# Performance work log

Hardware: AMD Instinct MI355X
Metric: run time of the kernel (lower is better)

Reference implementation:

```python
import jax, jax.numpy as jnp
import numpy as np

B, S, E, D = 4, 2048, 1024, 64  # batch, seq, embed_size, low-rank d; dv = E

def setup_inputs() -> dict:
    key = jax.random.key(0)
    ks = jax.random.split(key, 10)
    sc_e = 1.0 / np.sqrt(E)
    sc_d = 1.0 / np.sqrt(D)
    return {
        "x": jax.random.normal(ks[0], (B, S, E), jnp.float32),
        "y": jax.random.normal(ks[1], (B, S, E), jnp.float32),
        "Wq": jax.random.uniform(ks[2], (D, E), jnp.float32, -sc_e, sc_e),
        "bq": jax.random.uniform(ks[3], (D,), jnp.float32, -sc_e, sc_e),
        "Wk": jax.random.uniform(ks[4], (D, E), jnp.float32, -sc_e, sc_e),
        "bk": jax.random.uniform(ks[5], (D,), jnp.float32, -sc_e, sc_e),
        "WvR": jax.random.uniform(ks[6], (D, E), jnp.float32, -sc_e, sc_e),
        "bvR": jax.random.uniform(ks[7], (D,), jnp.float32, -sc_e, sc_e),
        "WvL": jax.random.uniform(ks[8], (E, D), jnp.float32, -sc_d, sc_d),
        "bvL": jax.random.uniform(ks[9], (E,), jnp.float32, -sc_d, sc_d),
    }

def reference(x, y, Wq, bq, Wk, bk, WvR, bvR, WvL, bvL):
    d = Wq.shape[0]
    Q = jnp.einsum('bse,de->bsd', x, Wq) + bq            # [B,S,D]
    K = jnp.einsum('bse,de->bsd', y, Wk) + bk            # [B,S,D]
    scores = jnp.einsum('bqd,bkd->bqk', Q, K) / jnp.sqrt(jnp.float32(d))
    # NOTE: original softmaxes over dim=1, i.e. the QUERY axis (faithful quirk)
    attn = jax.nn.softmax(scores, axis=1)                # [B,Sq,Sk]
    V = jnp.einsum('bsd,vd->bsv', jnp.einsum('bse,de->bsd', y, WvR) + bvR, WvL) + bvL  # [B,S,E]
    return jnp.einsum('bqk,bkv->bqv', attn, V)           # [B,S,E]
```

## Files before the change

kernel.cpp:

```cpp
#include <hip/hip_runtime.h>
#include <hip/hip_bf16.h>

#define DEV static __device__ __forceinline__
#define AS1 __attribute__((address_space(1)))
#define AS3 __attribute__((address_space(3)))

typedef __attribute__((ext_vector_type(8))) short bf16x8;
typedef __attribute__((ext_vector_type(4))) short bf16x4;
typedef __attribute__((ext_vector_type(4))) float f32x4;

constexpr int NB = 4;
constexpr int SS = 2048;
constexpr int EE = 1024;
constexpr int DD = 64;
constexpr int MTOT = NB * SS;

#define QSCALE (0.125f * 1.44269504088896340736f)

DEV short f2bf(float f) {
    union { float f; unsigned u; } v; v.f = f;
    unsigned u = v.u;
    u += 0x7FFFu + ((u >> 16) & 1u);
    return (short)(u >> 16);
}
DEV float bf2f(short h) {
    union { unsigned u; float f; } v; v.u = ((unsigned)(unsigned short)h) << 16;
    return v.f;
}
DEV unsigned pk2(float a, float b) {
    unsigned r;
    asm("v_cvt_pk_bf16_f32 %0, %1, %2" : "=v"(r) : "v"(a), "v"(b));
    return r;
}

DEV f32x4 mfma16(bf16x8 a, bf16x8 b, f32x4 c) {
    return __builtin_amdgcn_mfma_f32_16x16x32_bf16(a, b, c, 0, 0, 0);
}

DEV float redmax16(float v) {
    v = fmaxf(v, __shfl_xor(v, 1)); v = fmaxf(v, __shfl_xor(v, 2));
    v = fmaxf(v, __shfl_xor(v, 4)); v = fmaxf(v, __shfl_xor(v, 8));
    return v;
}
DEV float redsum16(float v) {
    v += __shfl_xor(v, 1); v += __shfl_xor(v, 2);
    v += __shfl_xor(v, 4); v += __shfl_xor(v, 8);
    return v;
}


__global__ __launch_bounds__(256) void k_prep(
    const float* __restrict__ Wq, const float* __restrict__ Wk,
    const float* __restrict__ Wv, const float* __restrict__ WvL,
    const float* __restrict__ bvL,
    short* __restrict__ Wqb, short* __restrict__ Wkb, short* __restrict__ Wvb,
    short* __restrict__ Wcat2)
{
    int g = blockIdx.x * 256 + threadIdx.x;
    if (g < 24576) {
        int mat = g >> 13;
        int c = g & 8191;
        int lane = c & 63;
        int fn = (c >> 6) & 3;
        int it = (c >> 8) & 7;
        int kq4 = c >> 11;
        int r = lane & 15, half = lane >> 4;
        int row = fn * 16 + r;
        int col = kq4 * 256 + it * 32 + half * 4;
        const float* W = (mat == 0) ? Wq : ((mat == 1) ? Wk : Wv);
        short* O = (mat == 0) ? Wqb : ((mat == 1) ? Wkb : Wvb);
        float s = (mat == 0) ? QSCALE : 1.0f;
        const float* Wp = W + (size_t)row * EE + col;
        float4 u = *(const float4*)(Wp);
        float4 v = *(const float4*)(Wp + 16);
        bf16x8 o;
        unsigned* ou = (unsigned*)&o;
        ou[0] = pk2(u.x * s, u.y * s);
        ou[1] = pk2(u.z * s, u.w * s);
        ou[2] = pk2(v.x * s, v.y * s);
        ou[3] = pk2(v.z * s, v.w * s);
        *(bf16x8*)(O + (size_t)c * 8) = o;
    } else {
        int i2 = g - 24576;
        int lane = i2 & 63;
        int ks = (i2 >> 6) % 5;
        int vt = i2 / 320;
        int r = lane & 15, h = lane >> 4;
        int v = vt * 16 + r;
        bf16x8 o;
        #pragma unroll
        for (int j = 0; j < 8; ++j) {
            int c = ks * 16 + (h & 1) * 8 + j;
            float val = (c < 64) ? WvL[(size_t)v * DD + c] : ((c == 64) ? bvL[v] : 0.f);
            o[j] = f2bf(val);
        }
        *(bf16x8*)(Wcat2 + ((size_t)(vt * 5 + ks) * 64 + lane) * 8) = o;
    }
}

__global__ __launch_bounds__(256) void k_proj(
    const float* __restrict__ x, const float* __restrict__ y,
    const short* __restrict__ Wqb, const short* __restrict__ Wkb,
    const short* __restrict__ Wvb,
    const float* __restrict__ bq, const float* __restrict__ bk,
    const float* __restrict__ bv,
    short* __restrict__ Qf, short* __restrict__ Kf, short* __restrict__ VF)
{
    const int tid = threadIdx.x, wave = tid >> 6, lane = tid & 63;
    const int r = lane & 15, half = lane >> 4;
    const int rb = blockIdx.x * 16;
    const bool isQ = (blockIdx.y == 0);
    const float* src = isQ ? x : y;
    const short* wA = isQ ? Wqb : Wkb;
    const int kq = wave * 256;

    __shared__ f32x4 red[4][8][64];

    f32x4 accA[4] = {}, accB[4] = {};
    const float* arow = src + (size_t)(rb + r) * EE + kq + half * 4;
    const short* wbase = wA + (size_t)wave * 16384 + lane * 8;
    const short* vbase = Wvb + (size_t)wave * 16384 + lane * 8;

    float4 af0[8], af1[8];
    #pragma unroll
    for (int it = 0; it < 8; ++it) {
        af0[it] = *(const float4*)(arow + it * 32);
        af1[it] = *(const float4*)(arow + it * 32 + 16);
    }

    bf16x8 bwc[4], bvc[4], bwn[4], bvn[4];
    #pragma unroll
    for (int n = 0; n < 4; ++n) bwc[n] = *(const bf16x8*)(wbase + n * 512);
    if (!isQ) {
        #pragma unroll
        for (int n = 0; n < 4; ++n) bvc[n] = *(const bf16x8*)(vbase + n * 512);
    }

    #pragma unroll
    for (int it = 0; it < 8; ++it) {
        if (it < 7) {
            #pragma unroll
            for (int n = 0; n < 4; ++n)
                bwn[n] = *(const bf16x8*)(wbase + ((it + 1) * 4 + n) * 512);
            if (!isQ) {
                #pragma unroll
                for (int n = 0; n < 4; ++n)
                    bvn[n] = *(const bf16x8*)(vbase + ((it + 1) * 4 + n) * 512);
            }
        }
        bf16x8 a;
        unsigned* au = (unsigned*)&a;
        au[0] = pk2(af0[it].x, af0[it].y);
        au[1] = pk2(af0[it].z, af0[it].w);
        au[2] = pk2(af1[it].x, af1[it].y);
        au[3] = pk2(af1[it].z, af1[it].w);
        #pragma unroll
        for (int n = 0; n < 4; ++n)
            accA[n] = mfma16(a, bwc[n], accA[n]);
        if (!isQ) {
            #pragma unroll
            for (int n = 0; n < 4; ++n)
                accB[n] = mfma16(a, bvc[n], accB[n]);
        }
        #pragma unroll
        for (int n = 0; n < 4; ++n) bwc[n] = bwn[n];
        if (!isQ) {
            #pragma unroll
            for (int n = 0; n < 4; ++n) bvc[n] = bvn[n];
        }
    }

    #pragma unroll
    for (int n = 0; n < 4; ++n) red[wave][n][lane] = accA[n];
    if (!isQ) {
        #pragma unroll
        for (int n = 0; n < 4; ++n) red[wave][4 + n][lane] = accB[n];
    }
    __syncthreads();

    const int n = wave;
    const int col = n * 16 + r;
    f32x4 s = red[0][n][lane];
    #pragma unroll
    for (int w = 1; w < 4; ++w) s += red[w][n][lane];
    float biasA = isQ ? (bq[col] * QSCALE) : bk[col];
    f32x4 t = {};
    float biasB = 0.f;
    if (!isQ) {
        t = red[0][4 + n][lane];
        #pragma unroll
        for (int w = 1; w < 4; ++w) t += red[w][4 + n][lane];
        biasB = bv[col];
    }
    __syncthreads();
    float* tlA = (float*)&red[0][0][0];
    float* tlB = tlA + 16 * 68;
    #pragma unroll
    for (int ri = 0; ri < 4; ++ri)
        tlA[(half * 4 + ri) * 68 + col] = s[ri] + biasA;
    if (!isQ) {
        #pragma unroll
        for (int ri = 0; ri < 4; ++ri)
            tlB[(half * 4 + ri) * 68 + col] = t[ri] + biasB;
    }
    __syncthreads();
    if (tid < 128) {
        int h2 = tid >> 6, l2 = tid & 63, r2 = l2 & 15, hh = l2 >> 4;
        const float* base = tlA + r2 * 68 + h2 * 32 + hh * 8;
        bf16x8 o;
        unsigned* ou = (unsigned*)&o;
        #pragma unroll
        for (int jj = 0; jj < 4; ++jj)
            ou[jj] = pk2(base[2 * jj], base[2 * jj + 1]);
        short* dst = (isQ ? Qf : Kf) + ((size_t)blockIdx.x * 2 + h2) * 512 + l2 * 8;
        *(bf16x8*)dst = o;
    } else if (!isQ) {
        int idx = tid - 128;
        int nn = idx >> 5, sub = idx & 31;
        int r2 = sub & 15, su = sub >> 4;
        int hbase = (rb & 16) ? 2 : 0;
        int lane2 = ((hbase + su) << 4) | r2;
        const float* base = tlB + (size_t)su * 8 * 68 + nn * 16 + r2;
        bf16x8 o;
        unsigned* ou = (unsigned*)&o;
        #pragma unroll
        for (int jj = 0; jj < 4; ++jj)
            ou[jj] = pk2(base[(2 * jj) * 68], base[(2 * jj + 1) * 68]);
        int batch = rb >> 11;
        int cg2 = (rb & 2047) >> 5;
        *(bf16x8*)(VF + (((size_t)batch * 64 + cg2) * 4 + nn) * 512 + lane2 * 8) = o;
    }
}

__global__ __launch_bounds__(512) void k_stats(
    const short* __restrict__ Qf, const short* __restrict__ Kf,
    float* __restrict__ Ml, float* __restrict__ Rl)
{
    const int tid = threadIdx.x, wave = tid >> 6, lane = tid & 63;
    const int r = lane & 15, half = lane >> 4;
    const int batch = blockIdx.y;
    const int kb = blockIdx.x * 16;

    __shared__ float smax[8][16], ssum[8][16];

    const short* kfp = Kf + ((size_t)(batch * 128 + (kb >> 4)) * 2) * 512 + lane * 8;
    bf16x8 kf0 = *(const bf16x8*)kfp;
    bf16x8 kf1 = *(const bf16x8*)(kfp + 512);

    const int qt0 = batch * 128 + wave * 16;
    f32x4 s[16];
    #pragma unroll
    for (int t = 0; t < 16; ++t) {
        const short* qp = Qf + ((size_t)(qt0 + t) * 2) * 512 + lane * 8;
        bf16x8 a0 = *(const bf16x8*)qp;
        bf16x8 a1 = *(const bf16x8*)(qp + 512);
        f32x4 c = {};
        c = mfma16(kf0, a0, c);
        c = mfma16(kf1, a1, c);
        s[t] = c;
    }
    f32x4 m4 = s[0];
    #pragma unroll
    for (int t = 1; t < 16; ++t) {
        #pragma unroll
        for (int ri = 0; ri < 4; ++ri) m4[ri] = fmaxf(m4[ri], s[t][ri]);
    }
    #pragma unroll
    for (int ri = 0; ri < 4; ++ri) m4[ri] = redmax16(m4[ri]);
    if (r == 0) {
        #pragma unroll
        for (int ri = 0; ri < 4; ++ri) smax[wave][half * 4 + ri] = m4[ri];
    }
    __syncthreads();
    f32x4 M;
    #pragma unroll
    for (int ri = 0; ri < 4; ++ri) {
        float v = smax[0][half * 4 + ri];
        #pragma unroll
        for (int w = 1; w < 8; ++w) v = fmaxf(v, smax[w][half * 4 + ri]);
        M[ri] = v;
    }
    f32x4 l4 = {};
    #pragma unroll
    for (int t = 0; t < 16; ++t)
        #pragma unroll
        for (int ri = 0; ri < 4; ++ri) l4[ri] += exp2f(s[t][ri] - M[ri]);
    #pragma unroll
    for (int ri = 0; ri < 4; ++ri) l4[ri] = redsum16(l4[ri]);
    if (r == 0) {
        #pragma unroll
        for (int ri = 0; ri < 4; ++ri) ssum[wave][half * 4 + ri] = l4[ri];
    }
    __syncthreads();
    if (wave == 0 && r == 0) {
        f32x4 rl;
        #pragma unroll
        for (int ri = 0; ri < 4; ++ri) {
            float v = 0.f;
            #pragma unroll
            for (int w = 0; w < 8; ++w) v += ssum[w][half * 4 + ri];
            rl[ri] = 1.0f / v;
        }
        *(f32x4*)(Ml + (size_t)batch * SS + kb + half * 4) = M;
        *(f32x4*)(Rl + (size_t)batch * SS + kb + half * 4) = rl;
    }
}

__global__ __launch_bounds__(512) void k_pvfuse(
    const short* __restrict__ Qf, const short* __restrict__ Kf,
    const short* __restrict__ VF,
    const float* __restrict__ Ml, const float* __restrict__ Rl,
    short* __restrict__ Tcat2)
{
    const int tid = threadIdx.x, wave = tid >> 6, lane = tid & 63;
    const int r = lane & 15, half = lane >> 4;
    const int bid = blockIdx.x;
    const int qt = (bid & 7) * 64 + (bid >> 3);
    const int batch = qt >> 7;
    const int kbase = wave * 256;

    __shared__ short pl[8][16][40];
    __shared__ f32x4 red2[8][5][64];
    __shared__ float tl2[16][84];

    const short* qp = Qf + (size_t)qt * 2 * 512 + lane * 8;
    bf16x8 qf0 = *(const bf16x8*)qp;
    bf16x8 qf1 = *(const bf16x8*)(qp + 512);
    bf16x8 ones;
    #pragma unroll
    for (int j = 0; j < 8; ++j) ones[j] = (r == 0) ? (short)0x3F80 : (short)0;

    const float* mlb = Ml + (size_t)batch * SS;
    const float* rlb = Rl + (size_t)batch * SS;
    const short* kfb = Kf + (size_t)batch * 128 * 1024;
    const short* vfb = VF + (size_t)batch * 64 * 4 * 512;

    f32x4 acc[5] = {};

    #pragma unroll 2
    for (int st = 0; st < 8; ++st) {
        const int kt = kbase + st * 32;
        const short* kp = kfb + (size_t)(kt >> 4) * 1024 + lane * 8;
        bf16x8 k00 = *(const bf16x8*)kp;
        bf16x8 k01 = *(const bf16x8*)(kp + 512);
        bf16x8 k10 = *(const bf16x8*)(kp + 1024);
        bf16x8 k11 = *(const bf16x8*)(kp + 1536);
        f32x4 s0 = {}, s1 = {};
        __builtin_amdgcn_s_setprio(1);
        s0 = mfma16(k00, qf0, s0); s0 = mfma16(k01, qf1, s0);
        s1 = mfma16(k10, qf0, s1); s1 = mfma16(k11, qf1, s1);
        __builtin_amdgcn_s_setprio(0);
        f32x4 m0 = *(const f32x4*)(mlb + kt + half * 4);
        f32x4 r0 = *(const f32x4*)(rlb + kt + half * 4);
        f32x4 m1 = *(const f32x4*)(mlb + kt + 16 + half * 4);
        f32x4 r1 = *(const f32x4*)(rlb + kt + 16 + half * 4);
        f32x4 p0, p1;
        #pragma unroll
        for (int ri = 0; ri < 4; ++ri) {
            p0[ri] = exp2f(s0[ri] - m0[ri]) * r0[ri];
            p1[ri] = exp2f(s1[ri] - m1[ri]) * r1[ri];
        }
        uint2 u0, u1;
        u0.x = pk2(p0[0], p0[1]); u0.y = pk2(p0[2], p0[3]);
        u1.x = pk2(p1[0], p1[1]); u1.y = pk2(p1[2], p1[3]);
        *(uint2*)&pl[wave][r][4 * half] = u0;
        *(uint2*)&pl[wave][r][16 + 4 * half] = u1;
        bf16x8 af = *(const bf16x8*)&pl[wave][r][half * 8];
        __builtin_amdgcn_s_setprio(1);
        #pragma unroll
        for (int nn = 0; nn < 4; ++nn) {
            bf16x8 vf = *(const bf16x8*)(vfb + ((size_t)(kt >> 5) * 4 + nn) * 512 + lane * 8);
            acc[nn] = mfma16(af, vf, acc[nn]);
        }
        acc[4] = mfma16(af, ones, acc[4]);
        __builtin_amdgcn_s_setprio(0);
    }

    #pragma unroll
    for (int nn = 0; nn < 5; ++nn) red2[wave][nn][lane] = acc[nn];
    __syncthreads();
    if (wave < 5) {
        int nn = wave;
        f32x4 v = red2[0][nn][lane];
        #pragma unroll
        for (int w = 1; w < 8; ++w) v += red2[w][nn][lane];
        #pragma unroll
        for (int ri = 0; ri < 4; ++ri) tl2[half * 4 + ri][nn * 16 + r] = v[ri];
    }
    __syncthreads();
    if (tid < 320) {
        int ks = tid >> 6;
        int l2 = tid & 63;
        int r2 = l2 & 15, h2 = l2 >> 4;
        bf16x8 o;
        #pragma unroll
        for (int j = 0; j < 8; ++j) {
            float v = tl2[r2][ks * 16 + (h2 & 1) * 8 + j];
            short hi = f2bf(v);
            o[j] = (h2 < 2) ? hi : f2bf(v - bf2f(hi));
        }
        *(bf16x8*)(Tcat2 + (((size_t)qt * 5 + ks) * 64 + l2) * 8) = o;
    }
}

__global__ __launch_bounds__(256) void k_gemm2(
    const short* __restrict__ Tcat2, const short* __restrict__ Wcat2,
    float* __restrict__ out)
{
    const int tid = threadIdx.x, wave = tid >> 6, lane = tid & 63;
    const int r = lane & 15, half = lane >> 4;
    const int wm = wave >> 1, wn = wave & 1;
    const int bid = blockIdx.x;
    const int w = (bid & 7) * 64 + (bid >> 3);
    const int qB = (w >> 3) * 128;
    const int vB = (w & 7) * 128;
    const int tA0 = qB / 16 + wm * 4;
    const int vt0 = vB / 16 + wn * 4;

    f32x4 acc[4][4] = {};
    #pragma unroll
    for (int ks = 0; ks < 5; ++ks) {
        bf16x8 a[4], b[4];
        #pragma unroll
        for (int i = 0; i < 4; ++i) {
            a[i] = *(const bf16x8*)(Tcat2 + ((size_t)(tA0 + i) * 5 + ks) * 512 + lane * 8);
            b[i] = *(const bf16x8*)(Wcat2 + ((size_t)(vt0 + i) * 5 + ks) * 512 + lane * 8);
        }
        #pragma unroll
        for (int mi = 0; mi < 4; ++mi)
            #pragma unroll
            for (int ni = 0; ni < 4; ++ni)
                acc[mi][ni] = mfma16(a[mi], b[ni], acc[mi][ni]);
    }

    const int r4 = half * 4;
    #pragma unroll
    for (int mi = 0; mi < 4; ++mi)
        #pragma unroll
        for (int ni = 0; ni < 4; ++ni)
            #pragma unroll
            for (int ri = 0; ri < 4; ++ri)
                out[(size_t)(qB + wm * 64 + mi * 16 + r4 + ri) * EE + vB + wn * 64 + ni * 16 + r] = acc[mi][ni][ri];
}

extern "C" void kernel_launch(void* const* d_in, const int* in_sizes, int n_in,
                              void* d_out, int out_size, void* d_ws, size_t ws_size,
                              hipStream_t stream) {
    (void)in_sizes; (void)n_in; (void)out_size; (void)ws_size;
    const float* x   = (const float*)d_in[0];
    const float* y   = (const float*)d_in[1];
    const float* Wq  = (const float*)d_in[2];
    const float* bq  = (const float*)d_in[3];
    const float* Wk  = (const float*)d_in[4];
    const float* bk  = (const float*)d_in[5];
    const float* WvR = (const float*)d_in[6];
    const float* bvR = (const float*)d_in[7];
    const float* WvL = (const float*)d_in[8];
    const float* bvL = (const float*)d_in[9];
    float* out = (float*)d_out;

    short* Qf    = (short*)d_ws;
    short* Kf    = Qf    + (size_t)MTOT * DD;
    short* VF    = Kf    + (size_t)MTOT * DD;
    short* Tcat2 = VF    + (size_t)MTOT * DD;
    short* Wqb   = Tcat2 + (size_t)(MTOT / 16) * 5 * 512;
    short* Wkb   = Wqb   + (size_t)DD * EE;
    short* Wvb   = Wkb   + (size_t)DD * EE;
    short* Wcat2 = Wvb   + (size_t)DD * EE;
    float* Ml    = (float*)(Wcat2 + (size_t)64 * 5 * 512);
    float* Rl    = Ml + MTOT;

    k_prep<<<dim3(176), 256, 0, stream>>>(Wq, Wk, WvR, WvL, bvL, Wqb, Wkb, Wvb, Wcat2);
    k_proj<<<dim3(MTOT / 16, 2), 256, 0, stream>>>(x, y, Wqb, Wkb, Wvb, bq, bk, bvR, Qf, Kf, VF);
    k_stats<<<dim3(SS / 16, NB), 512, 0, stream>>>(Qf, Kf, Ml, Rl);
    k_pvfuse<<<dim3(512), 512, 0, stream>>>(Qf, Kf, VF, Ml, Rl, Tcat2);
    k_gemm2<<<dim3(512), 256, 0, stream>>>(Tcat2, Wcat2, out);
}
```

Before: 64.29 us.

## Merge stats, PV and output GEMM into one persistent kernel with grid barriers

Fuses k_stats, k_pvfuse and k_gemm2 into a single 512-block kernel separated by atomic-counter grid barriers, which removes two kernel launches and their inter-kernel gaps. It also folds the softmax max and reciprocal sum into one log-sum-exp constant, so the PV stage loads one value per key instead of two and skips a multiply. The GEMM2 stage is re-tiled for 8 waves per block. The barrier relies on all 512 blocks being co-resident (launch_bounds 512,4 on 256 CUs), so there is a deadlock risk if occupancy falls short, and the spin waits add their own latency.

```diff
diff --git a/kernel.cpp b/kernel.cpp
--- a/kernel.cpp
+++ b/kernel.cpp
@@ -48,15 +48,28 @@
     return v;
 }
 
+DEV void gbar(unsigned* c) {
+    __syncthreads();
+    if (threadIdx.x == 0) {
+        __threadfence();
+        __hip_atomic_fetch_add(c, 1u, __ATOMIC_RELEASE, __HIP_MEMORY_SCOPE_AGENT);
+        while (__hip_atomic_load(c, __ATOMIC_ACQUIRE, __HIP_MEMORY_SCOPE_AGENT) < 512u)
+            __builtin_amdgcn_s_sleep(8);
+        __threadfence();
+    }
+    __syncthreads();
+}
+
 
 __global__ __launch_bounds__(256) void k_prep(
     const float* __restrict__ Wq, const float* __restrict__ Wk,
     const float* __restrict__ Wv, const float* __restrict__ WvL,
     const float* __restrict__ bvL,
     short* __restrict__ Wqb, short* __restrict__ Wkb, short* __restrict__ Wvb,
-    short* __restrict__ Wcat2)
+    short* __restrict__ Wcat2, unsigned* __restrict__ bar)
 {
     int g = blockIdx.x * 256 + threadIdx.x;
+    if (g == 0) { bar[0] = 0; bar[1] = 0; }
     if (g < 24576) {
         int mat = g >> 13;
         int c = g & 8191;
@@ -80,7 +93,7 @@
         ou[2] = pk2(v.x * s, v.y * s);
         ou[3] = pk2(v.z * s, v.w * s);
         *(bf16x8*)(O + (size_t)c * 8) = o;
-    } else {
+    } else if (g < 45056) {
         int i2 = g - 24576;
         int lane = i2 & 63;
         int ks = (i2 >> 6) % 5;
@@ -232,215 +245,209 @@
     }
 }
 
-__global__ __launch_bounds__(512) void k_stats(
-    const short* __restrict__ Qf, const short* __restrict__ Kf,
-    float* __restrict__ Ml, float* __restrict__ Rl)
-{
-    const int tid = threadIdx.x, wave = tid >> 6, lane = tid & 63;
-    const int r = lane & 15, half = lane >> 4;
-    const int batch = blockIdx.y;
-    const int kb = blockIdx.x * 16;
-
-    __shared__ float smax[8][16], ssum[8][16];
-
-    const short* kfp = Kf + ((size_t)(batch * 128 + (kb >> 4)) * 2) * 512 + lane * 8;
-    bf16x8 kf0 = *(const bf16x8*)kfp;
-    bf16x8 kf1 = *(const bf16x8*)(kfp + 512);
-
-    const int qt0 = batch * 128 + wave * 16;
-    f32x4 s[16];
-    #pragma unroll
-    for (int t = 0; t < 16; ++t) {
-        const short* qp = Qf + ((size_t)(qt0 + t) * 2) * 512 + lane * 8;
-        bf16x8 a0 = *(const bf16x8*)qp;
-        bf16x8 a1 = *(const bf16x8*)(qp + 512);
-        f32x4 c = {};
-        c = mfma16(kf0, a0, c);
-        c = mfma16(kf1, a1, c);
-        s[t] = c;
-    }
-    f32x4 m4 = s[0];
-    #pragma unroll
-    for (int t = 1; t < 16; ++t) {
-        #pragma unroll
-        for (int ri = 0; ri < 4; ++ri) m4[ri] = fmaxf(m4[ri], s[t][ri]);
-    }
-    #pragma unroll
-    for (int ri = 0; ri < 4; ++ri) m4[ri] = redmax16(m4[ri]);
-    if (r == 0) {
-        #pragma unroll
-        for (int ri = 0; ri < 4; ++ri) smax[wave][half * 4 + ri] = m4[ri];
-    }
-    __syncthreads();
-    f32x4 M;
-    #pragma unroll
-    for (int ri = 0; ri < 4; ++ri) {
-        float v = smax[0][half * 4 + ri];
-        #pragma unroll
-        for (int w = 1; w < 8; ++w) v = fmaxf(v, smax[w][half * 4 + ri]);
-        M[ri] = v;
-    }
-    f32x4 l4 = {};
-    #pragma unroll
-    for (int t = 0; t < 16; ++t)
-        #pragma unroll
-        for (int ri = 0; ri < 4; ++ri) l4[ri] += exp2f(s[t][ri] - M[ri]);
-    #pragma unroll
-    for (int ri = 0; ri < 4; ++ri) l4[ri] = redsum16(l4[ri]);
-    if (r == 0) {
-        #pragma unroll
-        for (int ri = 0; ri < 4; ++ri) ssum[wave][half * 4 + ri] = l4[ri];
-    }
-    __syncthreads();
-    if (wave == 0 && r == 0) {
-        f32x4 rl;
-        #pragma unroll
-        for (int ri = 0; ri < 4; ++ri) {
-            float v = 0.f;
-            #pragma unroll
-            for (int w = 0; w < 8; ++w) v += ssum[w][half * 4 + ri];
-            rl[ri] = 1.0f / v;
-        }
-        *(f32x4*)(Ml + (size_t)batch * SS + kb + half * 4) = M;
-        *(f32x4*)(Rl + (size_t)batch * SS + kb + half * 4) = rl;
-    }
-}
-
-__global__ __launch_bounds__(512) void k_pvfuse(
+__global__ __launch_bounds__(512, 4) void k_mega(
     const short* __restrict__ Qf, const short* __restrict__ Kf,
     const short* __restrict__ VF,
-    const float* __restrict__ Ml, const float* __restrict__ Rl,
-    short* __restrict__ Tcat2)
+    float* __restrict__ Cl,
+    const short* __restrict__ Wcat2,
+    short* __restrict__ Tcat2,
+    float* __restrict__ out,
+    unsigned* __restrict__ bar)
 {
     const int tid = threadIdx.x, wave = tid >> 6, lane = tid & 63;
     const int r = lane & 15, half = lane >> 4;
     const int bid = blockIdx.x;
-    const int qt = (bid & 7) * 64 + (bid >> 3);
-    const int batch = qt >> 7;
-    const int kbase = wave * 256;
-
-    __shared__ short pl[8][16][40];
-    __shared__ f32x4 red2[8][5][64];
-    __shared__ float tl2[16][84];
-
-    const short* qp = Qf + (size_t)qt * 2 * 512 + lane * 8;
-    bf16x8 qf0 = *(const bf16x8*)qp;
-    bf16x8 qf1 = *(const bf16x8*)(qp + 512);
-    bf16x8 ones;
-    #pragma unroll
-    for (int j = 0; j < 8; ++j) ones[j] = (r == 0) ? (short)0x3F80 : (short)0;
-
-    const float* mlb = Ml + (size_t)batch * SS;
-    const float* rlb = Rl + (size_t)batch * SS;
-    const short* kfb = Kf + (size_t)batch * 128 * 1024;
-    const short* vfb = VF + (size_t)batch * 64 * 4 * 512;
-
-    f32x4 acc[5] = {};
-
-    #pragma unroll 2
-    for (int st = 0; st < 8; ++st) {
-        const int kt = kbase + st * 32;
-        const short* kp = kfb + (size_t)(kt >> 4) * 1024 + lane * 8;
-        bf16x8 k00 = *(const bf16x8*)kp;
-        bf16x8 k01 = *(const bf16x8*)(kp + 512);
-        bf16x8 k10 = *(const bf16x8*)(kp + 1024);
-        bf16x8 k11 = *(const bf16x8*)(kp + 1536);
-        f32x4 s0 = {}, s1 = {};
-        __builtin_amdgcn_s_setprio(1);
-        s0 = mfma16(k00, qf0, s0); s0 = mfma16(k01, qf1, s0);
-        s1 = mfma16(k10, qf0, s1); s1 = mfma16(k11, qf1, s1);
-        __builtin_amdgcn_s_setprio(0);
-        f32x4 m0 = *(const f32x4*)(mlb + kt + half * 4);
-        f32x4 r0 = *(const f32x4*)(rlb + kt + half * 4);
-        f32x4 m1 = *(const f32x4*)(mlb + kt + 16 + half * 4);
-        f32x4 r1 = *(const f32x4*)(rlb + kt + 16 + half * 4);
-        f32x4 p0, p1;
+
+    __shared__ __align__(16) char smem[56576];
+    float* smax = (float*)smem;
+    float* ssum = smax + 128;
+    short (*pl)[16][40]   = (short(*)[16][40])smem;
+    f32x4 (*red2)[5][64]  = (f32x4(*)[5][64])(smem + 10240);
+    float (*tl2)[84]      = (float(*)[84])(smem + 51200);
+
+    {
+        const int batch = bid >> 7;
+        const int kb = (bid & 127) * 16;
+        const short* kfp = Kf + ((size_t)(batch * 128 + (kb >> 4)) * 2) * 512 + lane * 8;
+        bf16x8 kf0 = *(const bf16x8*)kfp;
+        bf16x8 kf1 = *(const bf16x8*)(kfp + 512);
+
+        const int qt0 = batch * 128 + wave * 16;
+        f32x4 s[16];
+        #pragma unroll
+        for (int t = 0; t < 16; ++t) {
+            const short* qp = Qf + ((size_t)(qt0 + t) * 2) * 512 + lane * 8;
+            bf16x8 a0 = *(const bf16x8*)qp;
+            bf16x8 a1 = *(const bf16x8*)(qp + 512);
+            f32x4 c = {};
+            c = mfma16(kf0, a0, c);
+            c = mfma16(kf1, a1, c);
+            s[t] = c;
+        }
+        f32x4 m4 = s[0];
+        #pragma unroll
+        for (int t = 1; t < 16; ++t) {
+            #pragma unroll
+            for (int ri = 0; ri < 4; ++ri) m4[ri] = fmaxf(m4[ri], s[t][ri]);
+        }
+        #pragma unroll
+        for (int ri = 0; ri < 4; ++ri) m4[ri] = redmax16(m4[ri]);
+        if (r == 0) {
+            #pragma unroll
+            for (int ri = 0; ri < 4; ++ri) smax[wave * 16 + half * 4 + ri] = m4[ri];
+        }
+        __syncthreads();
+        f32x4 M;
         #pragma unroll
         for (int ri = 0; ri < 4; ++ri) {
-            p0[ri] = exp2f(s0[ri] - m0[ri]) * r0[ri];
-            p1[ri] = exp2f(s1[ri] - m1[ri]) * r1[ri];
-        }
-        uint2 u0, u1;
-        u0.x = pk2(p0[0], p0[1]); u0.y = pk2(p0[2], p0[3]);
-        u1.x = pk2(p1[0], p1[1]); u1.y = pk2(p1[2], p1[3]);
-        *(uint2*)&pl[wave][r][4 * half] = u0;
-        *(uint2*)&pl[wave][r][16 + 4 * half] = u1;
-        bf16x8 af = *(const bf16x8*)&pl[wave][r][half * 8];
-        __builtin_amdgcn_s_setprio(1);
-        #pragma unroll
-        for (int nn = 0; nn < 4; ++nn) {
-            bf16x8 vf = *(const bf16x8*)(vfb + ((size_t)(kt >> 5) * 4 + nn) * 512 + lane * 8);
-            acc[nn] = mfma16(af, vf, acc[nn]);
-        }
-        acc[4] = mfma16(af, ones, acc[4]);
-        __builtin_amdgcn_s_setprio(0);
-    }
-
-    #pragma unroll
-    for (int nn = 0; nn < 5; ++nn) red2[wave][nn][lane] = acc[nn];
-    __syncthreads();
-    if (wave < 5) {
-        int nn = wave;
-        f32x4 v = red2[0][nn][lane];
-        #pragma unroll
-        for (int w = 1; w < 8; ++w) v += red2[w][nn][lane];
-        #pragma unroll
-        for (int ri = 0; ri < 4; ++ri) tl2[half * 4 + ri][nn * 16 + r] = v[ri];
-    }
-    __syncthreads();
-    if (tid < 320) {
-        int ks = tid >> 6;
-        int l2 = tid & 63;
-        int r2 = l2 & 15, h2 = l2 >> 4;
-        bf16x8 o;
-        #pragma unroll
-        for (int j = 0; j < 8; ++j) {
-            float v = tl2[r2][ks * 16 + (h2 & 1) * 8 + j];
-            short hi = f2bf(v);
-            o[j] = (h2 < 2) ? hi : f2bf(v - bf2f(hi));
-        }
-        *(bf16x8*)(Tcat2 + (((size_t)qt * 5 + ks) * 64 + l2) * 8) = o;
-    }
-}
-
-__global__ __launch_bounds__(256) void k_gemm2(
-    const short* __restrict__ Tcat2, const short* __restrict__ Wcat2,
-    float* __restrict__ out)
-{
-    const int tid = threadIdx.x, wave = tid >> 6, lane = tid & 63;
-    const int r = lane & 15, half = lane >> 4;
-    const int wm = wave >> 1, wn = wave & 1;
-    const int bid = blockIdx.x;
-    const int w = (bid & 7) * 64 + (bid >> 3);
-    const int qB = (w >> 3) * 128;
-    const int vB = (w & 7) * 128;
-    const int tA0 = qB / 16 + wm * 4;
-    const int vt0 = vB / 16 + wn * 4;
-
-    f32x4 acc[4][4] = {};
-    #pragma unroll
-    for (int ks = 0; ks < 5; ++ks) {
-        bf16x8 a[4], b[4];
-        #pragma unroll
-        for (int i = 0; i < 4; ++i) {
-            a[i] = *(const bf16x8*)(Tcat2 + ((size_t)(tA0 + i) * 5 + ks) * 512 + lane * 8);
-            b[i] = *(const bf16x8*)(Wcat2 + ((size_t)(vt0 + i) * 5 + ks) * 512 + lane * 8);
-        }
+            float v = smax[half * 4 + ri];
+            #pragma unroll
+            for (int w = 1; w < 8; ++w) v = fmaxf(v, smax[w * 16 + half * 4 + ri]);
+            M[ri] = v;
+        }
+        f32x4 l4 = {};
+        #pragma unroll
+        for (int t = 0; t < 16; ++t)
+            #pragma unroll
+            for (int ri = 0; ri < 4; ++ri) l4[ri] += exp2f(s[t][ri] - M[ri]);
+        #pragma unroll
+        for (int ri = 0; ri < 4; ++ri) l4[ri] = redsum16(l4[ri]);
+        if (r == 0) {
+            #pragma unroll
+            for (int ri = 0; ri < 4; ++ri) ssum[wave * 16 + half * 4 + ri] = l4[ri];
+        }
+        __syncthreads();
+        if (wave == 0 && r == 0) {
+            f32x4 C;
+            #pragma unroll
+            for (int ri = 0; ri < 4; ++ri) {
+                float v = 0.f;
+                #pragma unroll
+                for (int w = 0; w < 8; ++w) v += ssum[w * 16 + half * 4 + ri];
+                C[ri] = M[ri] + __log2f(v);
+            }
+            *(f32x4*)(Cl + (size_t)batch * SS + kb + half * 4) = C;
+        }
+    }
+    gbar(&bar[0]);
+
+    {
+        const int qt = (bid & 7) * 64 + (bid >> 3);
+        const int batch = qt >> 7;
+        const int kbase = wave * 256;
+
+        const short* qp = Qf + (size_t)qt * 2 * 512 + lane * 8;
+        bf16x8 qf0 = *(const bf16x8*)qp;
+        bf16x8 qf1 = *(const bf16x8*)(qp + 512);
+        bf16x8 ones;
+        #pragma unroll
+        for (int j = 0; j < 8; ++j) ones[j] = (r == 0) ? (short)0x3F80 : (short)0;
+
+        const float* clb = Cl + (size_t)batch * SS;
+        const short* kfb = Kf + (size_t)batch * 128 * 1024;
+        const short* vfb = VF + (size_t)batch * 64 * 4 * 512;
+
+        f32x4 acc[5] = {};
+
+        #pragma unroll 2
+        for (int st = 0; st < 8; ++st) {
+            const int kt = kbase + st * 32;
+            const short* kp = kfb + (size_t)(kt >> 4) * 1024 + lane * 8;
+            bf16x8 k00 = *(const bf16x8*)kp;
+            bf16x8 k01 = *(const bf16x8*)(kp + 512);
+            bf16x8 k10 = *(const bf16x8*)(kp + 1024);
+            bf16x8 k11 = *(const bf16x8*)(kp + 1536);
+            f32x4 s0 = {}, s1 = {};
+            __builtin_amdgcn_s_setprio(1);
+            s0 = mfma16(k00, qf0, s0); s0 = mfma16(k01, qf1, s0);
+            s1 = mfma16(k10, qf0, s1); s1 = mfma16(k11, qf1, s1);
+            __builtin_amdgcn_s_setprio(0);
+            f32x4 c0 = *(const f32x4*)(clb + kt + half * 4);
+            f32x4 c1 = *(const f32x4*)(clb + kt + 16 + half * 4);
+            f32x4 p0, p1;
+            #pragma unroll
+            for (int ri = 0; ri < 4; ++ri) {
+                p0[ri] = exp2f(s0[ri] - c0[ri]);
+                p1[ri] = exp2f(s1[ri] - c1[ri]);
+            }
+            uint2 u0, u1;
+            u0.x = pk2(p0[0], p0[1]); u0.y = pk2(p0[2], p0[3]);
+            u1.x = pk2(p1[0], p1[1]); u1.y = pk2(p1[2], p1[3]);
+            *(uint2*)&pl[wave][r][4 * half] = u0;
+            *(uint2*)&pl[wave][r][16 + 4 * half] = u1;
+            bf16x8 af = *(const bf16x8*)&pl[wave][r][half * 8];
+            __builtin_amdgcn_s_setprio(1);
+            #pragma unroll
+            for (int nn = 0; nn < 4; ++nn) {
+                bf16x8 vf = *(const bf16x8*)(vfb + ((size_t)(kt >> 5) * 4 + nn) * 512 + lane * 8);
+                acc[nn] = mfma16(af, vf, acc[nn]);
+            }
+            acc[4] = mfma16(af, ones, acc[4]);
+            __builtin_amdgcn_s_setprio(0);
+        }
+
+        #pragma unroll
+        for (int nn = 0; nn < 5; ++nn) red2[wave][nn][lane] = acc[nn];
+        __syncthreads();
+        if (wave < 5) {
+            int nn = wave;
+            f32x4 v = red2[0][nn][lane];
+            #pragma unroll
+            for (int w = 1; w < 8; ++w) v += red2[w][nn][lane];
+            #pragma unroll
+            for (int ri = 0; ri < 4; ++ri) tl2[half * 4 + ri][nn * 16 + r] = v[ri];
+        }
+        __syncthreads();
+        if (tid < 320) {
+            int ks = tid >> 6;
+            int l2 = tid & 63;
+            int r2 = l2 & 15, h2 = l2 >> 4;
+            bf16x8 o;
+            #pragma unroll
+            for (int j = 0; j < 8; ++j) {
+                float v = tl2[r2][ks * 16 + (h2 & 1) * 8 + j];
+                short hi = f2bf(v);
+                o[j] = (h2 < 2) ? hi : f2bf(v - bf2f(hi));
+            }
+            *(bf16x8*)(Tcat2 + (((size_t)qt * 5 + ks) * 64 + l2) * 8) = o;
+        }
+    }
+    gbar(&bar[1]);
+
+    {
+        const int wm = wave >> 2, wn = wave & 3;
+        const int w2 = (bid & 7) * 64 + (bid >> 3);
+        const int qB = (w2 >> 3) * 128;
+        const int vB = (w2 & 7) * 128;
+        const int tA0 = qB / 16 + wm * 4;
+        const int vt0 = vB / 16 + wn * 2;
+
+        f32x4 acc[4][2] = {};
+        #pragma unroll
+        for (int ks = 0; ks < 5; ++ks) {
+            bf16x8 a[4], b[2];
+            #pragma unroll
+            for (int i = 0; i < 4; ++i)
+                a[i] = *(const bf16x8*)(Tcat2 + ((size_t)(tA0 + i) * 5 + ks) * 512 + lane * 8);
+            #pragma unroll
+            for (int i = 0; i < 2; ++i)
+                b[i] = *(const bf16x8*)(Wcat2 + ((size_t)(vt0 + i) * 5 + ks) * 512 + lane * 8);
+            #pragma unroll
+            for (int mi = 0; mi < 4; ++mi)
+                #pragma unroll
+                for (int ni = 0; ni < 2; ++ni)
+                    acc[mi][ni] = mfma16(a[mi], b[ni], acc[mi][ni]);
+        }
+
+        const int r4 = half * 4;
         #pragma unroll
         for (int mi = 0; mi < 4; ++mi)
             #pragma unroll
-            for (int ni = 0; ni < 4; ++ni)
-                acc[mi][ni] = mfma16(a[mi], b[ni], acc[mi][ni]);
-    }
-
-    const int r4 = half * 4;
-    #pragma unroll
-    for (int mi = 0; mi < 4; ++mi)
-        #pragma unroll
-        for (int ni = 0; ni < 4; ++ni)
-            #pragma unroll
-            for (int ri = 0; ri < 4; ++ri)
-                out[(size_t)(qB + wm * 64 + mi * 16 + r4 + ri) * EE + vB + wn * 64 + ni * 16 + r] = acc[mi][ni][ri];
+            for (int ni = 0; ni < 2; ++ni)
+                #pragma unroll
+                for (int ri = 0; ri < 4; ++ri)
+                    out[(size_t)(qB + wm * 64 + mi * 16 + r4 + ri) * EE + vB + wn * 32 + ni * 16 + r] = acc[mi][ni][ri];
+    }
 }
 
 extern "C" void kernel_launch(void* const* d_in, const int* in_sizes, int n_in,
@@ -467,12 +474,10 @@
     short* Wkb   = Wqb   + (size_t)DD * EE;
     short* Wvb   = Wkb   + (size_t)DD * EE;
     short* Wcat2 = Wvb   + (size_t)DD * EE;
-    float* Ml    = (float*)(Wcat2 + (size_t)64 * 5 * 512);
-    float* Rl    = Ml + MTOT;
-
-    k_prep<<<dim3(176), 256, 0, stream>>>(Wq, Wk, WvR, WvL, bvL, Wqb, Wkb, Wvb, Wcat2);
+    float* Cl    = (float*)(Wcat2 + (size_t)64 * 5 * 512);
+    unsigned* bar = (unsigned*)(Cl + MTOT);
+
+    k_prep<<<dim3(176), 256, 0, stream>>>(Wq, Wk, WvR, WvL, bvL, Wqb, Wkb, Wvb, Wcat2, bar);
     k_proj<<<dim3(MTOT / 16, 2), 256, 0, stream>>>(x, y, Wqb, Wkb, Wvb, bq, bk, bvR, Qf, Kf, VF);
-    k_stats<<<dim3(SS / 16, NB), 512, 0, stream>>>(Qf, Kf, Ml, Rl);
-    k_pvfuse<<<dim3(512), 512, 0, stream>>>(Qf, Kf, VF, Ml, Rl, Tcat2);
-    k_gemm2<<<dim3(512), 256, 0, stream>>>(Tcat2, Wcat2, out);
-}
+    k_mega<<<dim3(512), 512, 0, stream>>>(Qf, Kf, VF, Cl, Wcat2, Tcat2, out, bar);
+}
```

Measured after the change: 158.8 us. 2.47x slower.
